# Kernel tuning notes

Measured on AMD Instinct MI355X. Metric: run time of the kernel, lower is better.

Reference implementation:

```python
import jax, jax.numpy as jnp
import numpy as np

B, N, D_IN, D_HID, D_OUT = 64, 512, 512, 512, 512


def setup_inputs() -> dict:
    key = jax.random.key(0)
    ks = jax.random.split(key, 8)
    gain = 0.02  # xavier_normal_ gain used in reset_parameters_xavier

    def xavier(k, fan_in, fan_out):
        std = gain * np.sqrt(2.0 / (fan_in + fan_out))
        return jax.random.normal(k, (fan_in, fan_out), dtype=jnp.float32) * std

    return {
        "batch_graph": jax.random.normal(ks[0], (B, N, D_IN), dtype=jnp.float32),
        "adj": jax.random.uniform(ks[1], (B, N, N), dtype=jnp.float32),
        "W1": xavier(ks[2], D_IN, D_HID),
        "b1": jnp.zeros((D_HID,), dtype=jnp.float32),
        "W2": xavier(ks[3], D_HID, D_HID),
        "b2": jnp.zeros((D_HID,), dtype=jnp.float32),
        "W3": xavier(ks[4], D_HID, D_OUT),
        "b3": jnp.zeros((D_OUT,), dtype=jnp.float32),
    }


def _normalize_adj(adj):
    # rowsum^-0.5 with inf -> 0 (original: torch.pow then isinf mask)
    rowsum = adj.sum(axis=1)                       # [B, N] (sum over dim 1, as in torch)
    safe = jnp.where(rowsum == 0, 1.0, rowsum)
    r = jnp.where(rowsum == 0, 0.0, safe ** -0.5)  # [B, N]
    # (adj @ D)^T @ D = D @ adj^T @ D with D = diag(r)
    return r[:, :, None] * jnp.swapaxes(adj, 1, 2) * r[:, None, :]


def reference(batch_graph, adj, W1, b1, W2, b2, W3, b3):
    # Block-diagonal big_adj @ big_graph == per-graph batched matmul.
    A = _normalize_adj(adj)  # [B, N, N]

    def gc(x, W, b):
        # support = x @ W ; output = A @ support + b
        return jnp.einsum('bij,bjd->bid', A, x @ W) + b

    # dropout is identity in eval mode (deterministic reference)
    x = jax.nn.relu(gc(batch_graph, W1, b1))
    x = jax.nn.relu(gc(x, W2, b2))
    return gc(x, W3, b3)  # [B, N, D_OUT]
```

## Files before the change

kernel.cpp:

```cpp
#include <hip/hip_runtime.h>
#include <cstdint>
#include <cstddef>

typedef _Float16 f16;
typedef _Float16 f16x4 __attribute__((ext_vector_type(4)));
typedef _Float16 f16x8 __attribute__((ext_vector_type(8)));
typedef float    f32x4 __attribute__((ext_vector_type(4)));

#define NB 64
#define NN 262144

__device__ __forceinline__ void gload_lds16(const void* g, void* l) {
    __builtin_amdgcn_global_load_lds(
        (const __attribute__((address_space(1))) void*)g,
        (__attribute__((address_space(3))) void*)l, 16, 0, 0);
}

__global__ __launch_bounds__(256, 4)
void k_pre(const float* __restrict__ X0, f16* __restrict__ X_h,
           const float* __restrict__ W1, const float* __restrict__ W2,
           const float* __restrict__ W3, f16* __restrict__ Wt,
           const float* __restrict__ adj, float* __restrict__ part) {
    __shared__ float t[64][65];
    const int bid = blockIdx.x, tid = threadIdx.x;

    if (bid < 1024) {
        int b = bid >> 4;
        int rr0 = (bid & 15) * 32 + (tid >> 7) * 16;
        int c4 = (tid & 127) * 4;
        const float* ab = adj + (size_t)b * NN + (size_t)rr0 * 512 + c4;
        f32x4 v[16];
        #pragma unroll
        for (int i = 0; i < 16; ++i)
            v[i] = *(const f32x4*)(ab + (size_t)i * 512);
        f32x4 s = ((v[0] + v[1]) + (v[2] + v[3])) + ((v[4] + v[5]) + (v[6] + v[7]))
                + ((v[8] + v[9]) + (v[10] + v[11])) + ((v[12] + v[13]) + (v[14] + v[15]));
        int ch2 = (bid & 15) * 2 + (tid >> 7);
        *(f32x4*)&part[((size_t)b * 32 + ch2) * 512 + c4] = s;
    } else {
        int cb = bid - 1024;
        float4 v[16];
        #pragma unroll
        for (int s = 0; s < 8; ++s) {
            size_t i = (((size_t)(cb + 1024 * s)) * 256 + tid) * 8;
            v[2 * s]     = *(const float4*)(X0 + i);
            v[2 * s + 1] = *(const float4*)(X0 + i + 4);
        }
        #pragma unroll
        for (int s = 0; s < 8; ++s) {
            size_t i = (((size_t)(cb + 1024 * s)) * 256 + tid) * 8;
            f16x8 o;
            o[0] = (f16)v[2*s].x;   o[1] = (f16)v[2*s].y;
            o[2] = (f16)v[2*s].z;   o[3] = (f16)v[2*s].w;
            o[4] = (f16)v[2*s+1].x; o[5] = (f16)v[2*s+1].y;
            o[6] = (f16)v[2*s+1].z; o[7] = (f16)v[2*s+1].w;
            *(f16x8*)(X_h + i) = o;
        }
        if (cb < 192) {
            int z = cb >> 6, rem = cb & 63;
            const float* W = z == 0 ? W1 : (z == 1 ? W2 : W3);
            f16* out = Wt + (size_t)z * NN;
            int k0 = (rem >> 3) * 64, d0 = (rem & 7) * 64;
            int c = tid & 63, r4 = tid >> 6;
            #pragma unroll
            for (int s = 0; s < 16; ++s) {
                int rr = r4 + s * 4;
                t[rr][c] = W[(size_t)(k0 + rr) * 512 + d0 + c];
            }
            __syncthreads();
            int kq = (tid & 15) * 4;
            int db = tid >> 4;
            #pragma unroll
            for (int s = 0; s < 4; ++s) {
                int dd = db + s * 16;
                f16x4 o;
                #pragma unroll
                for (int q = 0; q < 4; ++q)
                    o[q] = (f16)(64.f * t[kq + q][dd]);
                *(f16x4*)&out[(size_t)(d0 + dd) * 512 + k0 + kq] = o;
            }
        }
    }
}

__global__ void k_makeA(const float* __restrict__ adj, const float* __restrict__ part,
                        f16* __restrict__ A_h) {
    __shared__ float t[64][68];
    __shared__ float ri_s[64], rj_s[64];
    const int tid = threadIdx.x;
    int b = blockIdx.z;
    int i0 = blockIdx.y * 64, j0 = blockIdx.x * 64;
    const float* ab = adj + (size_t)b * NN;
    int trow = tid >> 4;
    int tc4  = (tid & 15) * 4;
    #pragma unroll
    for (int s = 0; s < 4; ++s) {
        int rr = trow + s * 16;
        *(f32x4*)&t[rr][tc4] = *(const f32x4*)&ab[(size_t)(j0 + rr) * 512 + i0 + tc4];
    }
    if (tid < 128) {
        int col = tid < 64 ? i0 + tid : j0 + tid - 64;
        const float* p = part + (size_t)b * 32 * 512 + col;
        float s = 0.f;
        #pragma unroll
        for (int ch = 0; ch < 32; ++ch) s += p[ch * 512];
        float rv = (s > 0.f) ? rsqrtf(s) : 0.f;
        if (tid < 64) ri_s[tid] = rv;
        else          rj_s[tid - 64] = rv;
    }
    __syncthreads();
    f16* Ab = A_h + (size_t)b * NN;
    int jq = (tid & 15) * 4;
    int ib = tid >> 4;
    #pragma unroll
    for (int s = 0; s < 4; ++s) {
        int ii = ib + s * 16;
        float ri = 16.f * ri_s[ii];
        f16x4 o;
        #pragma unroll
        for (int q = 0; q < 4; ++q)
            o[q] = (f16)(ri * t[jq + q][ii] * rj_s[jq + q]);
        *(f16x4*)&Ab[(size_t)(i0 + ii) * 512 + j0 + jq] = o;
    }
}

template<bool BIAS, bool RELU, bool OUTF32>
__global__ __launch_bounds__(256, 2)
void gemm_tn_ct(const f16* __restrict__ P, size_t pstr,
                const f16* __restrict__ Qt, size_t qstr,
                void* __restrict__ Cout, size_t cstr,
                const float* __restrict__ bias, float iscale, float oscale) {
    __shared__ __align__(16) f16 Plds[2][8192];
    __shared__ __align__(16) f16 Qlds[2][8192];

    const int tid  = threadIdx.x;
    const int lane = tid & 63;
    const int wid  = tid >> 6;
    const int wm   = wid >> 1;
    const int wn   = wid & 1;

    const int wg  = blockIdx.x;
    const int swz = (wg & 7) * 128 + (wg >> 3);
    const int b   = swz >> 4;
    const int tt  = swz & 15;
    const int m0  = (tt >> 2) * 128;
    const int n0  = (tt & 3) * 128;

    const f16* Pb = P + (size_t)b * pstr;
    const f16* Qb = Qt + (size_t)b * qstr;

    const int srow = tid >> 3;
    const int sswz = (tid & 7) ^ (srow & 7);

    const int fr  = lane & 15;
    const int fs  = lane >> 4;
    const int fx  = fr & 7;

    auto stage = [&](const f16* __restrict__ Gb, int row0, f16* lds, int k0) {
        #pragma unroll
        for (int r = 0; r < 4; ++r) {
            const f16* src = Gb + (size_t)(row0 + r * 32 + srow) * 512 + k0 + sswz * 8;
            gload_lds16(src, lds + r * 2048 + tid * 8);
        }
    };

    f32x4 acc[4][4] = {};

    stage(Pb, m0, &Plds[0][0], 0);
    stage(Qb, n0, &Qlds[0][0], 0);

    for (int t = 0; t < 8; ++t) {
        const int nb = t & 1;
        if (t < 7) {
            stage(Pb, m0, &Plds[nb ^ 1][0], (t + 1) * 64);
            stage(Qb, n0, &Qlds[nb ^ 1][0], (t + 1) * 64);
            asm volatile("s_waitcnt vmcnt(8)" ::: "memory");
        } else {
            asm volatile("s_waitcnt vmcnt(0)" ::: "memory");
        }
        __builtin_amdgcn_s_barrier();

        const f16* Pl = &Plds[nb][0];
        const f16* Ql = &Qlds[nb][0];
        #pragma unroll
        for (int krep = 0; krep < 2; ++krep) {
            const int sp = ((fs + krep * 4) ^ fx) * 8;
            f16x8 af[4], bf[4];
            #pragma unroll
            for (int mi = 0; mi < 4; ++mi)
                af[mi] = *(const f16x8*)&Pl[(wm * 64 + mi * 16 + fr) * 64 + sp];
            #pragma unroll
            for (int ni = 0; ni < 4; ++ni)
                bf[ni] = *(const f16x8*)&Ql[(wn * 64 + ni * 16 + fr) * 64 + sp];
            __builtin_amdgcn_s_setprio(1);
            #pragma unroll
            for (int mi = 0; mi < 4; ++mi)
                #pragma unroll
                for (int ni = 0; ni < 4; ++ni)
                    acc[mi][ni] = __builtin_amdgcn_mfma_f32_16x16x32_f16(
                        af[mi], bf[ni], acc[mi][ni], 0, 0, 0);
            __builtin_amdgcn_s_setprio(0);
        }
        asm volatile("s_waitcnt lgkmcnt(0)" ::: "memory");
        __builtin_amdgcn_sched_barrier(0);
        __builtin_amdgcn_s_barrier();
    }

    const int cmb = (lane >> 4) * 4;
    #pragma unroll
    for (int mi = 0; mi < 4; ++mi) {
        #pragma unroll
        for (int ni = 0; ni < 4; ++ni) {
            const int n = n0 + wn * 64 + ni * 16 + fr;
            const int m = m0 + wm * 64 + mi * 16 + cmb;
            float v[4];
            #pragma unroll
            for (int q = 0; q < 4; ++q) {
                float x = acc[mi][ni][q] * iscale;
                if (BIAS) x += bias[m + q];
                if (RELU) x = fmaxf(x, 0.f);
                v[q] = x * oscale;
            }
            if (OUTF32) {
                float* Cb = (float*)Cout + (size_t)b * cstr;
                f32x4 o; o[0] = v[0]; o[1] = v[1]; o[2] = v[2]; o[3] = v[3];
                *(f32x4*)&Cb[(size_t)n * 512 + m] = o;
            } else {
                f16* Cb = (f16*)Cout + (size_t)b * cstr;
                f16x4 o; o[0] = (f16)v[0]; o[1] = (f16)v[1]; o[2] = (f16)v[2]; o[3] = (f16)v[3];
                *(f16x4*)&Cb[(size_t)n * 512 + m] = o;
            }
        }
    }
}

extern "C" void kernel_launch(void* const* d_in, const int* in_sizes, int n_in,
                              void* d_out, int out_size, void* d_ws, size_t ws_size,
                              hipStream_t stream) {
    const float* X0  = (const float*)d_in[0];
    const float* adj = (const float*)d_in[1];
    const float* W1  = (const float*)d_in[2];
    const float* b1  = (const float*)d_in[3];
    const float* W2  = (const float*)d_in[4];
    const float* b2  = (const float*)d_in[5];
    const float* W3  = (const float*)d_in[6];
    const float* b3  = (const float*)d_in[7];

    uint8_t* ws = (uint8_t*)d_ws;
    f16* Wt1 = (f16*)(ws + 131072);
    f16* Wt2 = Wt1 + NN;
    f16* Wt3 = Wt2 + NN;
    f16* A_h = (f16*)(ws + 131072 + (size_t)3 * NN * 2);
    f16* X_h = A_h + (size_t)NB * NN;
    f16* S_t = X_h + (size_t)NB * NN;
    float* part = (float*)S_t;

    k_pre  <<<dim3(2048),     dim3(256), 0, stream>>>(X0, X_h, W1, W2, W3, Wt1, adj, part);
    k_makeA<<<dim3(8, 8, NB), dim3(256), 0, stream>>>(adj, part, A_h);

    dim3 gg(1024), gb(256);
    gemm_tn_ct<false, false, false><<<gg, gb, 0, stream>>>(X_h, (size_t)NN, Wt1, (size_t)0,  S_t, (size_t)NN, nullptr, 1.f, 1.f / 64.f);
    gemm_tn_ct<true,  true,  false><<<gg, gb, 0, stream>>>(S_t, (size_t)NN, A_h, (size_t)NN, X_h, (size_t)NN, b1, 1.f / 16.f, 1.f);
    gemm_tn_ct<false, false, false><<<gg, gb, 0, stream>>>(X_h, (size_t)NN, Wt2, (size_t)0,  S_t, (size_t)NN, nullptr, 1.f, 4.f);
    gemm_tn_ct<true,  true,  false><<<gg, gb, 0, stream>>>(S_t, (size_t)NN, A_h, (size_t)NN, X_h, (size_t)NN, b2, 1.f / 4096.f, 256.f);
    gemm_tn_ct<false, false, false><<<gg, gb, 0, stream>>>(X_h, (size_t)NN, Wt3, (size_t)0,  S_t, (size_t)NN, nullptr, 1.f, 1.f / 64.f);
    gemm_tn_ct<true,  false, true ><<<gg, gb, 0, stream>>>(S_t, (size_t)NN, A_h, (size_t)NN, d_out, (size_t)NN, b3, 1.f / 4096.f, 1.f);
}
```

Before: 234.4 us.

## Fuse fp32-to-fp16 input conversion into first GEMM and remap makeA grid

The separate pass that converted the fp32 node features to fp16 in the prologue kernel is removed. A new first-layer GEMM kernel now reads fp32 X directly into registers, converts it, and writes swizzled fp16 tiles into LDS, while the weight tile still uses async global-to-LDS loads. This avoids writing and re-reading a full fp16 copy of X. As a second change, the makeA grid becomes 1D with a mapping that groups each batch's tiles onto the same XCD. The fused loads are register-staged rather than async, which adds register pressure and may expose more latency in the first GEMM.

```diff
diff --git a/kernel.cpp b/kernel.cpp
--- a/kernel.cpp
+++ b/kernel.cpp
@@ -17,13 +17,11 @@
 }
 
 __global__ __launch_bounds__(256, 4)
-void k_pre(const float* __restrict__ X0, f16* __restrict__ X_h,
+void k_pre(const float* __restrict__ adj, float* __restrict__ part,
            const float* __restrict__ W1, const float* __restrict__ W2,
-           const float* __restrict__ W3, f16* __restrict__ Wt,
-           const float* __restrict__ adj, float* __restrict__ part) {
+           const float* __restrict__ W3, f16* __restrict__ Wt) {
     __shared__ float t[64][65];
     const int bid = blockIdx.x, tid = threadIdx.x;
-
     if (bid < 1024) {
         int b = bid >> 4;
         int rr0 = (bid & 15) * 32 + (tid >> 7) * 16;
@@ -39,46 +37,27 @@
         *(f32x4*)&part[((size_t)b * 32 + ch2) * 512 + c4] = s;
     } else {
         int cb = bid - 1024;
-        float4 v[16];
-        #pragma unroll
-        for (int s = 0; s < 8; ++s) {
-            size_t i = (((size_t)(cb + 1024 * s)) * 256 + tid) * 8;
-            v[2 * s]     = *(const float4*)(X0 + i);
-            v[2 * s + 1] = *(const float4*)(X0 + i + 4);
-        }
-        #pragma unroll
-        for (int s = 0; s < 8; ++s) {
-            size_t i = (((size_t)(cb + 1024 * s)) * 256 + tid) * 8;
-            f16x8 o;
-            o[0] = (f16)v[2*s].x;   o[1] = (f16)v[2*s].y;
-            o[2] = (f16)v[2*s].z;   o[3] = (f16)v[2*s].w;
-            o[4] = (f16)v[2*s+1].x; o[5] = (f16)v[2*s+1].y;
-            o[6] = (f16)v[2*s+1].z; o[7] = (f16)v[2*s+1].w;
-            *(f16x8*)(X_h + i) = o;
-        }
-        if (cb < 192) {
-            int z = cb >> 6, rem = cb & 63;
-            const float* W = z == 0 ? W1 : (z == 1 ? W2 : W3);
-            f16* out = Wt + (size_t)z * NN;
-            int k0 = (rem >> 3) * 64, d0 = (rem & 7) * 64;
-            int c = tid & 63, r4 = tid >> 6;
-            #pragma unroll
-            for (int s = 0; s < 16; ++s) {
-                int rr = r4 + s * 4;
-                t[rr][c] = W[(size_t)(k0 + rr) * 512 + d0 + c];
-            }
-            __syncthreads();
-            int kq = (tid & 15) * 4;
-            int db = tid >> 4;
-            #pragma unroll
-            for (int s = 0; s < 4; ++s) {
-                int dd = db + s * 16;
-                f16x4 o;
-                #pragma unroll
-                for (int q = 0; q < 4; ++q)
-                    o[q] = (f16)(64.f * t[kq + q][dd]);
-                *(f16x4*)&out[(size_t)(d0 + dd) * 512 + k0 + kq] = o;
-            }
+        int z = cb >> 6, rem = cb & 63;
+        const float* W = z == 0 ? W1 : (z == 1 ? W2 : W3);
+        f16* out = Wt + (size_t)z * NN;
+        int k0 = (rem >> 3) * 64, d0 = (rem & 7) * 64;
+        int c = tid & 63, r4 = tid >> 6;
+        #pragma unroll
+        for (int s = 0; s < 16; ++s) {
+            int rr = r4 + s * 4;
+            t[rr][c] = W[(size_t)(k0 + rr) * 512 + d0 + c];
+        }
+        __syncthreads();
+        int kq = (tid & 15) * 4;
+        int db = tid >> 4;
+        #pragma unroll
+        for (int s = 0; s < 4; ++s) {
+            int dd = db + s * 16;
+            f16x4 o;
+            #pragma unroll
+            for (int q = 0; q < 4; ++q)
+                o[q] = (f16)(64.f * t[kq + q][dd]);
+            *(f16x4*)&out[(size_t)(d0 + dd) * 512 + k0 + kq] = o;
         }
     }
 }
@@ -88,8 +67,11 @@
     __shared__ float t[64][68];
     __shared__ float ri_s[64], rj_s[64];
     const int tid = threadIdx.x;
-    int b = blockIdx.z;
-    int i0 = blockIdx.y * 64, j0 = blockIdx.x * 64;
+    const int bid = blockIdx.x;
+    const int xcd = bid & 7, loc = bid >> 3;
+    const int b = xcd * 8 + (loc >> 6);
+    const int tile = loc & 63;
+    const int i0 = (tile >> 3) * 64, j0 = (tile & 7) * 64;
     const float* ab = adj + (size_t)b * NN;
     int trow = tid >> 4;
     int tc4  = (tid & 15) * 4;
@@ -121,6 +103,124 @@
         for (int q = 0; q < 4; ++q)
             o[q] = (f16)(ri * t[jq + q][ii] * rj_s[jq + q]);
         *(f16x4*)&Ab[(size_t)(i0 + ii) * 512 + j0 + jq] = o;
+    }
+}
+
+__global__ __launch_bounds__(256, 2)
+void gemm1_cvt(const float* __restrict__ X0, const f16* __restrict__ Wt,
+               f16* __restrict__ S_t, float oscale) {
+    __shared__ __align__(16) f16 Plds[2][8192];
+    __shared__ __align__(16) f16 Qlds[2][8192];
+
+    const int tid  = threadIdx.x;
+    const int lane = tid & 63;
+    const int wid  = tid >> 6;
+    const int wm   = wid >> 1, wn = wid & 1;
+
+    const int wg  = blockIdx.x;
+    const int swz = (wg & 7) * 128 + (wg >> 3);
+    const int b   = swz >> 4;
+    const int tt  = swz & 15;
+    const int m0  = (tt >> 2) * 128;
+    const int n0  = (tt & 3) * 128;
+
+    const float* Pb = X0 + (size_t)b * NN;
+    const f16*   Qb = Wt;
+
+    const int srow = tid >> 3;
+    const int sswz = (tid & 7) ^ (srow & 7);
+    const int pr   = tid >> 3;
+    const int pc   = tid & 7;
+
+    const int fr = lane & 15, fs = lane >> 4, fx = fr & 7;
+
+    auto stageQ = [&](f16* lds, int k0) {
+        #pragma unroll
+        for (int r = 0; r < 4; ++r) {
+            const f16* src = Qb + (size_t)(n0 + r * 32 + srow) * 512 + k0 + sswz * 8;
+            gload_lds16(src, lds + r * 2048 + tid * 8);
+        }
+    };
+    float4 pv[4][2];
+    auto loadP = [&](int k0) {
+        #pragma unroll
+        for (int rep = 0; rep < 4; ++rep) {
+            const float* src = Pb + (size_t)(m0 + pr + rep * 32) * 512 + k0 + pc * 8;
+            pv[rep][0] = *(const float4*)src;
+            pv[rep][1] = *(const float4*)(src + 4);
+        }
+    };
+    auto writeP = [&](f16* lds) {
+        #pragma unroll
+        for (int rep = 0; rep < 4; ++rep) {
+            int r = pr + rep * 32;
+            f16x8 o;
+            o[0] = (f16)pv[rep][0].x; o[1] = (f16)pv[rep][0].y;
+            o[2] = (f16)pv[rep][0].z; o[3] = (f16)pv[rep][0].w;
+            o[4] = (f16)pv[rep][1].x; o[5] = (f16)pv[rep][1].y;
+            o[6] = (f16)pv[rep][1].z; o[7] = (f16)pv[rep][1].w;
+            *(f16x8*)(lds + r * 64 + (pc ^ (r & 7)) * 8) = o;
+        }
+    };
+
+    f32x4 acc[4][4] = {};
+
+    loadP(0);
+    stageQ(&Qlds[0][0], 0);
+    asm volatile("s_waitcnt vmcnt(0)" ::: "memory");
+    writeP(&Plds[0][0]);
+    asm volatile("s_waitcnt lgkmcnt(0)" ::: "memory");
+    __builtin_amdgcn_sched_barrier(0);
+    __builtin_amdgcn_s_barrier();
+
+    for (int t = 0; t < 8; ++t) {
+        const int nb = t & 1;
+        if (t < 7) {
+            loadP((t + 1) * 64);
+            stageQ(&Qlds[nb ^ 1][0], (t + 1) * 64);
+        }
+        const f16* Pl = &Plds[nb][0];
+        const f16* Ql = &Qlds[nb][0];
+        #pragma unroll
+        for (int krep = 0; krep < 2; ++krep) {
+            const int sp = ((fs + krep * 4) ^ fx) * 8;
+            f16x8 af[4], bf[4];
+            #pragma unroll
+            for (int mi = 0; mi < 4; ++mi)
+                af[mi] = *(const f16x8*)&Pl[(wm * 64 + mi * 16 + fr) * 64 + sp];
+            #pragma unroll
+            for (int ni = 0; ni < 4; ++ni)
+                bf[ni] = *(const f16x8*)&Ql[(wn * 64 + ni * 16 + fr) * 64 + sp];
+            __builtin_amdgcn_s_setprio(1);
+            #pragma unroll
+            for (int mi = 0; mi < 4; ++mi)
+                #pragma unroll
+                for (int ni = 0; ni < 4; ++ni)
+                    acc[mi][ni] = __builtin_amdgcn_mfma_f32_16x16x32_f16(
+                        af[mi], bf[ni], acc[mi][ni], 0, 0, 0);
+            __builtin_amdgcn_s_setprio(0);
+        }
+        if (t < 7) {
+            asm volatile("s_waitcnt vmcnt(0)" ::: "memory");
+            writeP(&Plds[nb ^ 1][0]);
+        }
+        asm volatile("s_waitcnt lgkmcnt(0)" ::: "memory");
+        __builtin_amdgcn_sched_barrier(0);
+        __builtin_amdgcn_s_barrier();
+    }
+
+    const int cmb = (lane >> 4) * 4;
+    #pragma unroll
+    for (int mi = 0; mi < 4; ++mi) {
+        #pragma unroll
+        for (int ni = 0; ni < 4; ++ni) {
+            const int n = n0 + wn * 64 + ni * 16 + fr;
+            const int m = m0 + wm * 64 + mi * 16 + cmb;
+            f16x4 o;
+            #pragma unroll
+            for (int q = 0; q < 4; ++q) o[q] = (f16)(acc[mi][ni][q] * oscale);
+            *(f16x4*)&S_t[(size_t)b * NN + (size_t)n * 512 + m] = o;
+        }
     }
 }
 
@@ -251,18 +351,19 @@
     f16* Wt2 = Wt1 + NN;
     f16* Wt3 = Wt2 + NN;
     f16* A_h = (f16*)(ws + 131072 + (size_t)3 * NN * 2);
-    f16* X_h = A_h + (size_t)NB * NN;
-    f16* S_t = X_h + (size_t)NB * NN;
+    f16* Xa  = A_h + (size_t)NB * NN;
+    f16* S_t = Xa + (size_t)NB * NN;
     float* part = (float*)S_t;
 
-    k_pre  <<<dim3(2048),     dim3(256), 0, stream>>>(X0, X_h, W1, W2, W3, Wt1, adj, part);
-    k_makeA<<<dim3(8, 8, NB), dim3(256), 0, stream>>>(adj, part, A_h);
+    k_pre  <<<dim3(1216), dim3(256), 0, stream>>>(adj, part, W1, W2, W3, Wt1);
+    k_makeA<<<dim3(4096), dim3(256), 0, stream>>>(adj, part, A_h);
+
+    gemm1_cvt<<<dim3(1024), dim3(256), 0, stream>>>(X0, Wt1, S_t, 1.f / 64.f);
 
     dim3 gg(1024), gb(256);
-    gemm_tn_ct<false, false, false><<<gg, gb, 0, stream>>>(X_h, (size_t)NN, Wt1, (size_t)0,  S_t, (size_t)NN, nullptr, 1.f, 1.f / 64.f);
-    gemm_tn_ct<true,  true,  false><<<gg, gb, 0, stream>>>(S_t, (size_t)NN, A_h, (size_t)NN, X_h, (size_t)NN, b1, 1.f / 16.f, 1.f);
-    gemm_tn_ct<false, false, false><<<gg, gb, 0, stream>>>(X_h, (size_t)NN, Wt2, (size_t)0,  S_t, (size_t)NN, nullptr, 1.f, 4.f);
-    gemm_tn_ct<true,  true,  false><<<gg, gb, 0, stream>>>(S_t, (size_t)NN, A_h, (size_t)NN, X_h, (size_t)NN, b2, 1.f / 4096.f, 256.f);
-    gemm_tn_ct<false, false, false><<<gg, gb, 0, stream>>>(X_h, (size_t)NN, Wt3, (size_t)0,  S_t, (size_t)NN, nullptr, 1.f, 1.f / 64.f);
+    gemm_tn_ct<true,  true,  false><<<gg, gb, 0, stream>>>(S_t, (size_t)NN, A_h, (size_t)NN, Xa, (size_t)NN, b1, 1.f / 16.f, 1.f);
+    gemm_tn_ct<false, false, false><<<gg, gb, 0, stream>>>(Xa, (size_t)NN, Wt2, (size_t)0,  S_t, (size_t)NN, nullptr, 1.f, 4.f);
+    gemm_tn_ct<true,  true,  false><<<gg, gb, 0, stream>>>(S_t, (size_t)NN, A_h, (size_t)NN, Xa, (size_t)NN, b2, 1.f / 4096.f, 256.f);
+    gemm_tn_ct<false, false, false><<<gg, gb, 0, stream>>>(Xa, (size_t)NN, Wt3, (size_t)0,  S_t, (size_t)NN, nullptr, 1.f, 1.f / 64.f);
     gemm_tn_ct<true,  false, true ><<<gg, gb, 0, stream>>>(S_t, (size_t)NN, A_h, (size_t)NN, d_out, (size_t)NN, b3, 1.f / 4096.f, 1.f);
 }
```

Measured after the change: 227.4 us. -3.0%, faster.
